# Optimization experiments

Hardware: AMD Instinct MI355X
Metric: run time of the kernel (lower is better)

## Reference

```python
import jax, jax.numpy as jnp
import numpy as np

N, C, H, W = 32, 512, 32, 32
K = 64  # num_clusters
D_OUT = 256


def _l2n(v, axis):
    # torch F.normalize: v / max(||v||, 1e-12)
    n = jnp.linalg.norm(v, axis=axis, keepdims=True)
    return v / jnp.maximum(n, 1e-12)


def _bn(v, gamma, beta):
    # BatchNorm1d, training mode (batch stats, biased variance), eps=1e-5
    m = v.mean(axis=0)
    var = ((v - m) ** 2).mean(axis=0)
    return (v - m) / jnp.sqrt(var + 1e-5) * gamma + beta


def setup_inputs() -> dict:
    key = jax.random.key(0)
    ks = jax.random.split(key, 5)
    x = jax.random.normal(ks[0], (N, C, H, W), dtype=jnp.float32)
    conv_w = jax.random.normal(ks[1], (K, C), dtype=jnp.float32) * 0.05
    centroids = jax.random.uniform(ks[2], (K, C), dtype=jnp.float32)
    hidden_w = jax.random.normal(ks[3], (K * C, D_OUT), dtype=jnp.float32) / jnp.sqrt(jnp.float32(C))
    gating_w = jax.random.normal(ks[4], (D_OUT, D_OUT), dtype=jnp.float32) / jnp.sqrt(jnp.float32(D_OUT))
    return {
        "x": x,
        "conv_w": conv_w,
        "centroids": centroids,
        "hidden_w": hidden_w,
        "bn2_gamma": jnp.ones((D_OUT,), jnp.float32),
        "bn2_beta": jnp.zeros((D_OUT,), jnp.float32),
        "gating_w": gating_w,
        "gbn_gamma": jnp.ones((D_OUT,), jnp.float32),
        "gbn_beta": jnp.zeros((D_OUT,), jnp.float32),
    }


def reference(x, conv_w, centroids, hidden_w, bn2_gamma, bn2_beta, gating_w, gbn_gamma, gbn_beta):
    n = x.shape[0]
    # descriptor-wise L2 normalization over channel dim
    x = _l2n(x, axis=1)                                  # [N,C,H,W]
    xf = x.reshape(n, x.shape[1], -1)                    # [N,C,S]
    # 1x1 conv -> soft assignment, softmax over clusters
    sa = jnp.einsum('ncs,kc->nks', xf, conv_w)           # [N,K,S]
    sa = jax.nn.softmax(sa, axis=1)
    # matmul-form NetVLAD: sum_s a[n,k,s]*(x[n,c,s]-cent[k,c])
    vlad = jnp.einsum('nks,ncs->nkc', sa, xf) \
         - sa.sum(axis=-1)[..., None] * centroids[None]  # [N,K,C]
    vlad = _l2n(vlad, axis=2)                            # intra-normalization
    vlad = _l2n(vlad.reshape(n, -1), axis=1)             # [N,K*C]
    v = vlad @ hidden_w                                  # [N,256]
    v = _bn(v, bn2_gamma, bn2_beta)
    # context gating
    gates = jax.nn.sigmoid(_bn(v @ gating_w, gbn_gamma, gbn_beta))
    return v * gates
```

## Files before the change

kernel.cpp:

```cpp
#include <hip/hip_runtime.h>
#include <math.h>

static constexpr int Nb = 32;
static constexpr int Cc = 512;
static constexpr int Ss = 1024;
static constexpr int Kk = 64;
static constexpr int Dd = 256;

typedef __attribute__((ext_vector_type(8))) short bf16x8;
typedef __attribute__((ext_vector_type(4))) float f32x4;
typedef __attribute__((ext_vector_type(4))) unsigned int u32x4;

union FragU { u32x4 u; bf16x8 h; };

__device__ __forceinline__ unsigned hi_pack(float x0, float x1) {
    return __builtin_amdgcn_perm(__float_as_uint(x1), __float_as_uint(x0), 0x07060302u);
}
__device__ __forceinline__ float trunc_hi(float x) {
    return __uint_as_float(__float_as_uint(x) & 0xFFFF0000u);
}
__device__ __forceinline__ void split8(const float* xv, FragU& bh, FragU& bl) {
#pragma unroll
    for (int p = 0; p < 4; ++p) {
        bh.u[p] = hi_pack(xv[2*p], xv[2*p+1]);
        float l0 = xv[2*p]   - trunc_hi(xv[2*p]);
        float l1 = xv[2*p+1] - trunc_hi(xv[2*p+1]);
        bl.u[p] = hi_pack(l0, l1);
    }
}

__device__ __forceinline__ void gload_lds16(const float* g, void* l) {
    __builtin_amdgcn_global_load_lds(
        (const __attribute__((address_space(1))) void*)g,
        (__attribute__((address_space(3))) void*)l, 16, 0, 0);
}

__global__ __launch_bounds__(256) void kprep_cw(
    const float* __restrict__ cw, short* __restrict__ cwh, short* __restrict__ cwl)
{
    int t = blockIdx.x * 256 + threadIdx.x;
    float4 v = *(const float4*)&cw[4 * (size_t)t];
    unsigned h0 = hi_pack(v.x, v.y), h1 = hi_pack(v.z, v.w);
    float l0 = v.x - trunc_hi(v.x), l1 = v.y - trunc_hi(v.y);
    float l2 = v.z - trunc_hi(v.z), l3 = v.w - trunc_hi(v.w);
    unsigned g0 = hi_pack(l0, l1), g1 = hi_pack(l2, l3);
    ((uint2*)cwh)[t] = make_uint2(h0, h1);
    ((uint2*)cwl)[t] = make_uint2(g0, g1);
}

__global__ __launch_bounds__(512) void k1_sa(
    const float* __restrict__ x, const short* __restrict__ cw_hi,
    const short* __restrict__ cw_lo, short* __restrict__ a_hi,
    short* __restrict__ a_lo, float* __restrict__ asum_part)
{
    __shared__ float xt[2 * 64 * 64];
    __shared__ f32x4 comb[4][64][4];
    __shared__ float combq[4][64];

    const int tid = threadIdx.x;
    const int w = tid >> 6, lane = tid & 63;
    const int wq = w & 3, wh = w >> 2;
    const int l15 = lane & 15, lg = lane >> 4;
    const int n = blockIdx.y, s0 = blockIdx.x * 64;

    const float* xg = x + ((size_t)n * Cc) * Ss + s0 + 4 * (tid & 15);
    const int st_c = tid >> 4;

    auto GL = [&](int b, int ct) {
#pragma unroll
        for (int r = 0; r < 2; ++r) {
            const float* src = xg + (size_t)(ct * 64 + st_c + 32 * r) * Ss;
            void* dst = (char*)xt + b * 16384 + 1024 * w + 8192 * r;
            gload_lds16(src, dst);
        }
    };

    f32x4 zero4 = {0.f, 0.f, 0.f, 0.f};
    f32x4 acc[4] = {zero4, zero4, zero4, zero4};
    float ssq = 0.f;

    const int sl = 16 * wq + l15;
    const int cb = wh * 32 + 8 * lg;

    GL(0, 0);
    __syncthreads();

    for (int ct = 0; ct < 8; ++ct) {
        const int b = ct & 1;
        if (ct < 7) GL(b ^ 1, ct + 1);

        float xv[8];
#pragma unroll
        for (int j = 0; j < 8; ++j) xv[j] = xt[b * 4096 + (cb + j) * 64 + sl];
#pragma unroll
        for (int j = 0; j < 8; ++j) ssq += xv[j] * xv[j];
        FragU bh, bl;
        split8(xv, bh, bl);

        const int cg = ct * 64 + cb;
#pragma unroll
        for (int m = 0; m < 4; ++m) {
            FragU ah, al;
            const int row = 16 * m + l15;
            ah.u = *(const u32x4*)&cw_hi[(size_t)row * Cc + cg];
            al.u = *(const u32x4*)&cw_lo[(size_t)row * Cc + cg];
            acc[m] = __builtin_amdgcn_mfma_f32_16x16x32_bf16(al.h, bh.h, acc[m], 0, 0, 0);
            acc[m] = __builtin_amdgcn_mfma_f32_16x16x32_bf16(ah.h, bl.h, acc[m], 0, 0, 0);
            acc[m] = __builtin_amdgcn_mfma_f32_16x16x32_bf16(ah.h, bh.h, acc[m], 0, 0, 0);
        }
        __syncthreads();
    }

    if (wh == 1) {
#pragma unroll
        for (int m = 0; m < 4; ++m) comb[wq][lane][m] = acc[m];
        combq[wq][lane] = ssq;
    }
    __syncthreads();
    if (wh == 1) return;

#pragma unroll
    for (int m = 0; m < 4; ++m) acc[m] += comb[wq][lane][m];
    ssq += combq[wq][lane];

    ssq += __shfl_xor(ssq, 16);
    ssq += __shfl_xor(ssq, 32);
    const float inv = 1.f / fmaxf(sqrtf(ssq), 1e-12f);

    float sv[4][4];
    float mmax = -1e30f;
#pragma unroll
    for (int m = 0; m < 4; ++m)
#pragma unroll
        for (int r = 0; r < 4; ++r) {
            sv[m][r] = acc[m][r] * inv;
            mmax = fmaxf(mmax, sv[m][r]);
        }
    mmax = fmaxf(mmax, __shfl_xor(mmax, 16));
    mmax = fmaxf(mmax, __shfl_xor(mmax, 32));
    float den = 0.f;
#pragma unroll
    for (int m = 0; m < 4; ++m)
#pragma unroll
        for (int r = 0; r < 4; ++r) {
            sv[m][r] = expf(sv[m][r] - mmax);
            den += sv[m][r];
        }
    den += __shfl_xor(den, 16);
    den += __shfl_xor(den, 32);
    const float rinv = 1.f / den;

    const int scol = s0 + sl;
#pragma unroll
    for (int m = 0; m < 4; ++m)
#pragma unroll
        for (int r = 0; r < 4; ++r) {
            const float a = sv[m][r] * rinv;
            const int k = 16 * m + 4 * lg + r;
            float t = a;
            t += __shfl_xor(t, 1); t += __shfl_xor(t, 2);
            t += __shfl_xor(t, 4); t += __shfl_xor(t, 8);
            if (l15 == 0)
                asum_part[((size_t)(n * Kk + k) << 6) + blockIdx.x * 4 + wq] = t;
            const float av = a * inv;
            const unsigned u = __float_as_uint(av);
            const float hv = __uint_as_float(u & 0xFFFF0000u);
            const size_t idx = (size_t)(n * Kk + k) * Ss + scol;
            a_hi[idx] = (short)(u >> 16);
            a_lo[idx] = (short)(__float_as_uint(av - hv) >> 16);
        }
}

__global__ __launch_bounds__(256) void kasum(
    const float* __restrict__ asum_part, float* __restrict__ asum)
{
    int row = blockIdx.x * 256 + threadIdx.x;
    const float* p = &asum_part[(size_t)row << 6];
    float s = 0.f;
#pragma unroll
    for (int i = 0; i < 16; ++i) {
        float4 v = *(const float4*)&p[4 * i];
        s += v.x + v.y + v.z + v.w;
    }
    asum[row] = s;
}

__global__ __launch_bounds__(512) void k2_vlad(
    const float* __restrict__ x, const short* __restrict__ a_hi,
    const short* __restrict__ a_lo, const float* __restrict__ centroids,
    const float* __restrict__ asum, float* __restrict__ vp0,
    float* __restrict__ vp1)
{
    __shared__ f32x4 comb[4][64][4];
    __shared__ float asum_l[64];

    const int tid = threadIdx.x;
    const int w = tid >> 6, lane = tid & 63;
    const int wq = w & 3, wh = w >> 2;
    const int l15 = lane & 15, lg = lane >> 4;
    const int n = blockIdx.x, cp = blockIdx.y, sh = blockIdx.z;

    if (sh == 1 && tid < 64) asum_l[tid] = asum[n * Kk + tid];

    f32x4 zero4 = {0.f, 0.f, 0.f, 0.f};
    f32x4 acc[4] = {zero4, zero4, zero4, zero4};

    const int c = cp * 64 + 16 * wq + l15;
    const int sbase = sh * 512 + wh * 256;
    const float* xrow = x + (size_t)(n * Cc + c) * Ss + sbase;
    const short* ahb = a_hi + (size_t)n * Kk * Ss + sbase;
    const short* alb = a_lo + (size_t)n * Kk * Ss + sbase;

#pragma unroll 2
    for (int st = 0; st < 8; ++st) {
        const int so = st * 32 + 8 * lg;
        float4 xa = *(const float4*)&xrow[so];
        float4 xb = *(const float4*)&xrow[so + 4];
        float xv[8] = {xa.x, xa.y, xa.z, xa.w, xb.x, xb.y, xb.z, xb.w};
        FragU bh, bl;
        split8(xv, bh, bl);
#pragma unroll
        for (int m = 0; m < 4; ++m) {
            FragU ah, al;
            const size_t ao = (size_t)(16 * m + l15) * Ss + so;
            ah.u = *(const u32x4*)&ahb[ao];
            al.u = *(const u32x4*)&alb[ao];
            acc[m] = __builtin_amdgcn_mfma_f32_16x16x32_bf16(al.h, bh.h, acc[m], 0, 0, 0);
            acc[m] = __builtin_amdgcn_mfma_f32_16x16x32_bf16(ah.h, bl.h, acc[m], 0, 0, 0);
            acc[m] = __builtin_amdgcn_mfma_f32_16x16x32_bf16(ah.h, bh.h, acc[m], 0, 0, 0);
        }
    }

    if (wh == 1) {
#pragma unroll
        for (int m = 0; m < 4; ++m) comb[wq][lane][m] = acc[m];
    }
    __syncthreads();
    if (wh == 1) return;

    float* dst = sh ? vp1 : vp0;
#pragma unroll
    for (int m = 0; m < 4; ++m) {
        acc[m] += comb[wq][lane][m];
#pragma unroll
        for (int r = 0; r < 4; ++r) {
            const int k = 16 * m + 4 * lg + r;
            float val = acc[m][r];
            if (sh == 1) val -= asum_l[k] * centroids[(size_t)k * Cc + c];
            dst[(size_t)(n * Kk + k) * Cc + c] = val;
        }
    }
}

__global__ __launch_bounds__(512) void k3a_norm(
    float* __restrict__ vlad, const float* __restrict__ vp1,
    float* __restrict__ nrm)
{
    const int tid = threadIdx.x;
    const int w = tid >> 6, lane = tid & 63;
    const int n = blockIdx.x, kg = blockIdx.y;
    const int row = (n * Kk) + kg * 8 + w;
    const size_t base = (size_t)row * Cc + lane * 8;

    float4 v0 = *(const float4*)&vlad[base];
    float4 v1 = *(const float4*)&vlad[base + 4];
    float4 u0 = *(const float4*)&vp1[base];
    float4 u1 = *(const float4*)&vp1[base + 4];
    v0.x += u0.x; v0.y += u0.y; v0.z += u0.z; v0.w += u0.w;
    v1.x += u1.x; v1.y += u1.y; v1.z += u1.z; v1.w += u1.w;
    *(float4*)&vlad[base] = v0;
    *(float4*)&vlad[base + 4] = v1;
    float ssq = v0.x*v0.x + v0.y*v0.y + v0.z*v0.z + v0.w*v0.w
              + v1.x*v1.x + v1.y*v1.y + v1.z*v1.z + v1.w*v1.w;
#pragma unroll
    for (int off = 32; off >= 1; off >>= 1) ssq += __shfl_xor(ssq, off);
    if (lane == 0) nrm[row] = sqrtf(ssq);
}

__global__ __launch_bounds__(64) void k3b_scale(
    const float* __restrict__ nrm, float* __restrict__ scale)
{
    const int n = blockIdx.x, k = threadIdx.x;
    float r = nrm[n * Kk + k];
    float rn = r / fmaxf(r, 1e-12f);
    float p = rn * rn;
#pragma unroll
    for (int off = 32; off >= 1; off >>= 1) p += __shfl_xor(p, off);
    float g = sqrtf(p);
    scale[n * Kk + k] = 1.f / (fmaxf(r, 1e-12f) * fmaxf(g, 1e-12f));
}

__global__ __launch_bounds__(512) void k4_hidden(
    const float* __restrict__ vlad, const float* __restrict__ scale,
    const float* __restrict__ hw, float* __restrict__ vpart)
{
    __shared__ float vl[128][36];
    __shared__ float scale_l[32];
    const int tid = threadIdx.x;
    const int kc0 = blockIdx.x * 128;
    const int k = kc0 >> 9;
    if (tid < 32) scale_l[tid] = scale[tid * Kk + k];
    __syncthreads();
#pragma unroll
    for (int i = 0; i < 8; ++i) {
        int idx = tid + i * 512;
        int nn = idx >> 7, kcl = idx & 127;
        vl[kcl][nn] = vlad[(size_t)nn * (Kk * Cc) + kc0 + kcl] * scale_l[nn];
    }
    __syncthreads();

    const int dq = tid & 63, nq = tid >> 6;
    float acc[4][4];
#pragma unroll
    for (int i = 0; i < 4; ++i)
#pragma unroll
        for (int j = 0; j < 4; ++j) acc[i][j] = 0.f;

    for (int kcl = 0; kcl < 128; ++kcl) {
        const float4 v0 = *(const float4*)&vl[kcl][nq * 4];
        const float* wrow = &hw[(size_t)(kc0 + kcl) * Dd + dq];
#pragma unroll
        for (int dd = 0; dd < 4; ++dd) {
            float w = wrow[64 * dd];
            acc[dd][0] += w * v0.x; acc[dd][1] += w * v0.y;
            acc[dd][2] += w * v0.z; acc[dd][3] += w * v0.w;
        }
    }
#pragma unroll
    for (int dd = 0; dd < 4; ++dd)
#pragma unroll
        for (int j = 0; j < 4; ++j)
            vpart[((size_t)blockIdx.x * Nb + nq * 4 + j) * Dd + dq + 64 * dd] = acc[dd][j];
}

__global__ __launch_bounds__(128) void k5a_reduce(
    const float* __restrict__ vpart, float* __restrict__ v)
{
    int flat = blockIdx.x * 128 + threadIdx.x;
    float s = 0.f;
#pragma unroll 8
    for (int ch = 0; ch < 256; ++ch) s += vpart[(size_t)ch * (Nb * Dd) + flat];
    v[flat] = s;
}

__global__ __launch_bounds__(256) void k5b_bn(
    const float* __restrict__ v, const float* __restrict__ gamma,
    const float* __restrict__ beta, float* __restrict__ v_bn)
{
    const int d = threadIdx.x;
    float vals[Nb];
    float s1 = 0.f;
#pragma unroll
    for (int n = 0; n < Nb; ++n) {
        vals[n] = v[n * Dd + d];
        s1 += vals[n];
    }
    float m = s1 * (1.f / Nb);
    float var = 0.f;
#pragma unroll
    for (int n = 0; n < Nb; ++n) {
        float t = vals[n] - m;
        var += t * t;
    }
    var *= (1.f / Nb);
    float inv = rsqrtf(var + 1e-5f);
    float g = gamma[d], b = beta[d];
#pragma unroll
    for (int n = 0; n < Nb; ++n)
        v_bn[n * Dd + d] = (vals[n] - m) * inv * g + b;
}

__global__ __launch_bounds__(256) void k5c_gate(
    const float* __restrict__ v_bn, const float* __restrict__ gw,
    float* __restrict__ g_raw)
{
    __shared__ float vb[Dd];
    const int n = blockIdx.x, d = threadIdx.x;
    vb[d] = v_bn[n * Dd + d];
    __syncthreads();
    float acc = 0.f;
#pragma unroll 8
    for (int c = 0; c < Dd; ++c) acc += vb[c] * gw[c * Dd + d];
    g_raw[n * Dd + d] = acc;
}

__global__ __launch_bounds__(256) void k5d_out(
    const float* __restrict__ g_raw, const float* __restrict__ v_bn,
    const float* __restrict__ ggamma, const float* __restrict__ gbeta,
    float* __restrict__ out)
{
    const int d = threadIdx.x;
    float vals[Nb];
    float s1 = 0.f;
#pragma unroll
    for (int n = 0; n < Nb; ++n) {
        vals[n] = g_raw[n * Dd + d];
        s1 += vals[n];
    }
    float m = s1 * (1.f / Nb);
    float var = 0.f;
#pragma unroll
    for (int n = 0; n < Nb; ++n) {
        float t = vals[n] - m;
        var += t * t;
    }
    var *= (1.f / Nb);
    float inv = rsqrtf(var + 1e-5f);
    float g = ggamma[d], b = gbeta[d];
#pragma unroll
    for (int n = 0; n < Nb; ++n) {
        float t = (vals[n] - m) * inv * g + b;
        float sg = 1.f / (1.f + expf(-t));
        out[n * Dd + d] = v_bn[n * Dd + d] * sg;
    }
}

extern "C" void kernel_launch(void* const* d_in, const int* in_sizes, int n_in,
                              void* d_out, int out_size, void* d_ws, size_t ws_size,
                              hipStream_t stream)
{
    const float* x         = (const float*)d_in[0];
    const float* conv_w    = (const float*)d_in[1];
    const float* centroids = (const float*)d_in[2];
    const float* hidden_w  = (const float*)d_in[3];
    const float* bn2_gamma = (const float*)d_in[4];
    const float* bn2_beta  = (const float*)d_in[5];
    const float* gating_w  = (const float*)d_in[6];
    const float* gbn_gamma = (const float*)d_in[7];
    const float* gbn_beta  = (const float*)d_in[8];
    float* out = (float*)d_out;

    char* B = (char*)d_ws;
    short* a_hi      = (short*)(B);
    short* a_lo      = (short*)(B + (4u << 20));
    float* vp0       = (float*)(B + (8u << 20));
    float* vp1       = (float*)(B + (12u << 20));
    short* cw_hi     = (short*)(B + (16u << 20));
    short* cw_lo     = (short*)(B + (16u << 20) + 65536u);
    float* asum_part = (float*)(B + (16u << 20) + 131072u);
    float* asum      = (float*)(B + (16u << 20) + 655360u);
    float* nrm       = asum + 2048;
    float* scale     = nrm + 2048;
    float* v         = scale + 2048;
    float* v_bn      = v + 8192;
    float* g_raw     = v_bn + 8192;
    float* vpart     = (float*)B;

    kprep_cw<<<32, 256, 0, stream>>>(conv_w, cw_hi, cw_lo);
    k1_sa<<<dim3(16, 32), 512, 0, stream>>>(x, cw_hi, cw_lo, a_hi, a_lo, asum_part);
    kasum<<<8, 256, 0, stream>>>(asum_part, asum);
    k2_vlad<<<dim3(32, 8, 2), 512, 0, stream>>>(x, a_hi, a_lo, centroids, asum, vp0, vp1);
    k3a_norm<<<dim3(32, 8), 512, 0, stream>>>(vp0, vp1, nrm);
    k3b_scale<<<32, 64, 0, stream>>>(nrm, scale);
    k4_hidden<<<256, 512, 0, stream>>>(vp0, scale, hidden_w, vpart);
    k5a_reduce<<<64, 128, 0, stream>>>(vpart, v);
    k5b_bn<<<1, 256, 0, stream>>>(v, bn2_gamma, bn2_beta, v_bn);
    k5c_gate<<<32, 256, 0, stream>>>(v_bn, gating_w, g_raw);
    k5d_out<<<1, 256, 0, stream>>>(g_raw, v_bn, gbn_gamma, gbn_beta, out);
}
```

Before: 143.6 us.

## Repartition soft-assignment and VLAD kernels for more blocks; fuse BN into gating GEMV

k1_sa now gives each block 32 spatial columns instead of 64, and each wave owns one 16-cluster row tile rather than all four. This doubles the grid, and the per-column softmax max and sum are combined across waves through shared memory. It adds an XOR swizzle on the LDS tile to avoid bank conflicts. k2_vlad takes 32 channels per block across 4 spatial slices, doubling its grid, and reduces three partial accumulators through LDS. The single-block BatchNorm kernel is folded into the gating GEMV, which removes one launch but has every block recompute the column statistics redundantly.

```diff
diff --git a/kernel.cpp b/kernel.cpp
--- a/kernel.cpp
+++ b/kernel.cpp
@@ -53,34 +53,31 @@
     const short* __restrict__ cw_lo, short* __restrict__ a_hi,
     short* __restrict__ a_lo, float* __restrict__ asum_part)
 {
-    __shared__ float xt[2 * 64 * 64];
-    __shared__ f32x4 comb[4][64][4];
-    __shared__ float combq[4][64];
+    __shared__ float xt[2 * 2048];
+    __shared__ float redm[4][32];
+    __shared__ float reds[4][32];
 
     const int tid = threadIdx.x;
     const int w = tid >> 6, lane = tid & 63;
-    const int wq = w & 3, wh = w >> 2;
+    const int m = w & 3, sg = w >> 2;
     const int l15 = lane & 15, lg = lane >> 4;
-    const int n = blockIdx.y, s0 = blockIdx.x * 64;
-
-    const float* xg = x + ((size_t)n * Cc) * Ss + s0 + 4 * (tid & 15);
-    const int st_c = tid >> 4;
+    const int n = blockIdx.y, s0 = blockIdx.x * 32;
+
+    const float* xg = x + (size_t)n * Cc * Ss + s0
+                    + 4 * ((tid & 7) ^ (4 * ((tid >> 6) & 1)));
+    const int st_c = tid >> 3;
 
     auto GL = [&](int b, int ct) {
-#pragma unroll
-        for (int r = 0; r < 2; ++r) {
-            const float* src = xg + (size_t)(ct * 64 + st_c + 32 * r) * Ss;
-            void* dst = (char*)xt + b * 16384 + 1024 * w + 8192 * r;
-            gload_lds16(src, dst);
-        }
+        const float* src = xg + (size_t)(ct * 64 + st_c) * Ss;
+        void* dst = (char*)xt + b * 8192 + 1024 * w;
+        gload_lds16(src, dst);
     };
 
-    f32x4 zero4 = {0.f, 0.f, 0.f, 0.f};
-    f32x4 acc[4] = {zero4, zero4, zero4, zero4};
+    f32x4 acc = {0.f, 0.f, 0.f, 0.f};
     float ssq = 0.f;
 
-    const int sl = 16 * wq + l15;
-    const int cb = wh * 32 + 8 * lg;
+    const int xcol = (16 * sg + l15) ^ (16 * (lg & 1));
+    const int row16 = 16 * m + l15;
 
     GL(0, 0);
     __syncthreads();
@@ -88,87 +85,75 @@
     for (int ct = 0; ct < 8; ++ct) {
         const int b = ct & 1;
         if (ct < 7) GL(b ^ 1, ct + 1);
-
-        float xv[8];
-#pragma unroll
-        for (int j = 0; j < 8; ++j) xv[j] = xt[b * 4096 + (cb + j) * 64 + sl];
-#pragma unroll
-        for (int j = 0; j < 8; ++j) ssq += xv[j] * xv[j];
-        FragU bh, bl;
-        split8(xv, bh, bl);
-
-        const int cg = ct * 64 + cb;
-#pragma unroll
-        for (int m = 0; m < 4; ++m) {
+#pragma unroll
+        for (int ks = 0; ks < 2; ++ks) {
+            const int cb = ks * 32 + 8 * lg;
+            float xv[8];
+#pragma unroll
+            for (int j = 0; j < 8; ++j) xv[j] = xt[b * 2048 + (cb + j) * 32 + xcol];
+#pragma unroll
+            for (int j = 0; j < 8; ++j) ssq += xv[j] * xv[j];
+            FragU bh, bl;
+            split8(xv, bh, bl);
             FragU ah, al;
-            const int row = 16 * m + l15;
-            ah.u = *(const u32x4*)&cw_hi[(size_t)row * Cc + cg];
-            al.u = *(const u32x4*)&cw_lo[(size_t)row * Cc + cg];
-            acc[m] = __builtin_amdgcn_mfma_f32_16x16x32_bf16(al.h, bh.h, acc[m], 0, 0, 0);
-            acc[m] = __builtin_amdgcn_mfma_f32_16x16x32_bf16(ah.h, bl.h, acc[m], 0, 0, 0);
-            acc[m] = __builtin_amdgcn_mfma_f32_16x16x32_bf16(ah.h, bh.h, acc[m], 0, 0, 0);
+            const int cg = ct * 64 + cb;
+            ah.u = *(const u32x4*)&cw_hi[(size_t)row16 * Cc + cg];
+            al.u = *(const u32x4*)&cw_lo[(size_t)row16 * Cc + cg];
+            acc = __builtin_amdgcn_mfma_f32_16x16x32_bf16(al.h, bh.h, acc, 0, 0, 0);
+            acc = __builtin_amdgcn_mfma_f32_16x16x32_bf16(ah.h, bl.h, acc, 0, 0, 0);
+            acc = __builtin_amdgcn_mfma_f32_16x16x32_bf16(ah.h, bh.h, acc, 0, 0, 0);
         }
         __syncthreads();
     }
-
-    if (wh == 1) {
-#pragma unroll
-        for (int m = 0; m < 4; ++m) comb[wq][lane][m] = acc[m];
-        combq[wq][lane] = ssq;
-    }
-    __syncthreads();
-    if (wh == 1) return;
-
-#pragma unroll
-    for (int m = 0; m < 4; ++m) acc[m] += comb[wq][lane][m];
-    ssq += combq[wq][lane];
 
     ssq += __shfl_xor(ssq, 16);
     ssq += __shfl_xor(ssq, 32);
     const float inv = 1.f / fmaxf(sqrtf(ssq), 1e-12f);
 
-    float sv[4][4];
+    const int sl = 16 * sg + l15;
+    float sv[4];
     float mmax = -1e30f;
 #pragma unroll
-    for (int m = 0; m < 4; ++m)
-#pragma unroll
-        for (int r = 0; r < 4; ++r) {
-            sv[m][r] = acc[m][r] * inv;
-            mmax = fmaxf(mmax, sv[m][r]);
-        }
+    for (int r = 0; r < 4; ++r) {
+        sv[r] = acc[r] * inv;
+        mmax = fmaxf(mmax, sv[r]);
+    }
     mmax = fmaxf(mmax, __shfl_xor(mmax, 16));
     mmax = fmaxf(mmax, __shfl_xor(mmax, 32));
+    if (lg == 0) redm[m][sl] = mmax;
+    __syncthreads();
+    mmax = fmaxf(fmaxf(redm[0][sl], redm[1][sl]),
+                 fmaxf(redm[2][sl], redm[3][sl]));
     float den = 0.f;
 #pragma unroll
-    for (int m = 0; m < 4; ++m)
-#pragma unroll
-        for (int r = 0; r < 4; ++r) {
-            sv[m][r] = expf(sv[m][r] - mmax);
-            den += sv[m][r];
-        }
+    for (int r = 0; r < 4; ++r) {
+        sv[r] = expf(sv[r] - mmax);
+        den += sv[r];
+    }
     den += __shfl_xor(den, 16);
     den += __shfl_xor(den, 32);
+    if (lg == 0) reds[m][sl] = den;
+    __syncthreads();
+    den = reds[0][sl] + reds[1][sl] + reds[2][sl] + reds[3][sl];
     const float rinv = 1.f / den;
 
     const int scol = s0 + sl;
 #pragma unroll
-    for (int m = 0; m < 4; ++m)
-#pragma unroll
-        for (int r = 0; r < 4; ++r) {
-            const float a = sv[m][r] * rinv;
-            const int k = 16 * m + 4 * lg + r;
-            float t = a;
-            t += __shfl_xor(t, 1); t += __shfl_xor(t, 2);
-            t += __shfl_xor(t, 4); t += __shfl_xor(t, 8);
-            if (l15 == 0)
-                asum_part[((size_t)(n * Kk + k) << 6) + blockIdx.x * 4 + wq] = t;
-            const float av = a * inv;
-            const unsigned u = __float_as_uint(av);
-            const float hv = __uint_as_float(u & 0xFFFF0000u);
-            const size_t idx = (size_t)(n * Kk + k) * Ss + scol;
-            a_hi[idx] = (short)(u >> 16);
-            a_lo[idx] = (short)(__float_as_uint(av - hv) >> 16);
-        }
+    for (int r = 0; r < 4; ++r) {
+        const float a = sv[r] * rinv;
+        const int k = 16 * m + 4 * lg + r;
+        float t = a;
+        t += __shfl_xor(t, 1); t += __shfl_xor(t, 2);
+        t += __shfl_xor(t, 4); t += __shfl_xor(t, 8);
+        if (l15 == 0)
+            asum_part[((size_t)(n * Kk + k) << 6) + blockIdx.x * 2 + sg] = t;
+        const float av = a * inv;
+        const unsigned u = __float_as_uint(av);
+        const float hv = __uint_as_float(u & 0xFFFF0000u);
+        const size_t idx = (size_t)(n * Kk + k) * Ss + scol;
+        a_hi[idx] = (short)(u >> 16);
+        a_lo[idx] = (short)(__float_as_uint(av - hv) >> 16);
+    }
 }
 
 __global__ __launch_bounds__(256) void kasum(
@@ -191,12 +176,12 @@
     const float* __restrict__ asum, float* __restrict__ vp0,
     float* __restrict__ vp1)
 {
-    __shared__ f32x4 comb[4][64][4];
+    __shared__ f32x4 comb[3][2][64][4];
     __shared__ float asum_l[64];
 
     const int tid = threadIdx.x;
     const int w = tid >> 6, lane = tid & 63;
-    const int wq = w & 3, wh = w >> 2;
+    const int wq = w & 1, wh = w >> 1;
     const int l15 = lane & 15, lg = lane >> 4;
     const int n = blockIdx.x, cp = blockIdx.y, sh = blockIdx.z;
 
@@ -205,14 +190,14 @@
     f32x4 zero4 = {0.f, 0.f, 0.f, 0.f};
     f32x4 acc[4] = {zero4, zero4, zero4, zero4};
 
-    const int c = cp * 64 + 16 * wq + l15;
-    const int sbase = sh * 512 + wh * 256;
+    const int c = cp * 32 + 16 * wq + l15;
+    const int sbase = sh * 512 + wh * 128;
     const float* xrow = x + (size_t)(n * Cc + c) * Ss + sbase;
     const short* ahb = a_hi + (size_t)n * Kk * Ss + sbase;
     const short* alb = a_lo + (size_t)n * Kk * Ss + sbase;
 
 #pragma unroll 2
-    for (int st = 0; st < 8; ++st) {
+    for (int st = 0; st < 4; ++st) {
         const int so = st * 32 + 8 * lg;
         float4 xa = *(const float4*)&xrow[so];
         float4 xb = *(const float4*)&xrow[so + 4];
@@ -231,17 +216,19 @@
         }
     }
 
-    if (wh == 1) {
-#pragma unroll
-        for (int m = 0; m < 4; ++m) comb[wq][lane][m] = acc[m];
-    }
-    __syncthreads();
-    if (wh == 1) return;
+    if (wh) {
+#pragma unroll
+        for (int m = 0; m < 4; ++m) comb[wh - 1][wq][lane][m] = acc[m];
+    }
+    __syncthreads();
+    if (wh) return;
 
     float* dst = sh ? vp1 : vp0;
 #pragma unroll
     for (int m = 0; m < 4; ++m) {
-        acc[m] += comb[wq][lane][m];
+        acc[m] += comb[0][wq][lane][m];
+        acc[m] += comb[1][wq][lane][m];
+        acc[m] += comb[2][wq][lane][m];
 #pragma unroll
         for (int r = 0; r < 4; ++r) {
             const int k = 16 * m + 4 * lg + r;
@@ -343,41 +330,31 @@
     v[flat] = s;
 }
 
-__global__ __launch_bounds__(256) void k5b_bn(
+__global__ __launch_bounds__(256) void k5bc_gate(
     const float* __restrict__ v, const float* __restrict__ gamma,
-    const float* __restrict__ beta, float* __restrict__ v_bn)
-{
-    const int d = threadIdx.x;
-    float vals[Nb];
+    const float* __restrict__ beta, const float* __restrict__ gw,
+    float* __restrict__ v_bn, float* __restrict__ g_raw)
+{
+    __shared__ float vb[Dd];
+    const int n = blockIdx.x, d = threadIdx.x;
+
     float s1 = 0.f;
-#pragma unroll
-    for (int n = 0; n < Nb; ++n) {
-        vals[n] = v[n * Dd + d];
-        s1 += vals[n];
-    }
-    float m = s1 * (1.f / Nb);
+#pragma unroll 8
+    for (int i = 0; i < Nb; ++i) s1 += v[i * Dd + d];
+    float mean = s1 * (1.f / Nb);
     float var = 0.f;
-#pragma unroll
-    for (int n = 0; n < Nb; ++n) {
-        float t = vals[n] - m;
+#pragma unroll 8
+    for (int i = 0; i < Nb; ++i) {
+        float t = v[i * Dd + d] - mean;
         var += t * t;
     }
     var *= (1.f / Nb);
     float inv = rsqrtf(var + 1e-5f);
-    float g = gamma[d], b = beta[d];
-#pragma unroll
-    for (int n = 0; n < Nb; ++n)
-        v_bn[n * Dd + d] = (vals[n] - m) * inv * g + b;
-}
-
-__global__ __launch_bounds__(256) void k5c_gate(
-    const float* __restrict__ v_bn, const float* __restrict__ gw,
-    float* __restrict__ g_raw)
-{
-    __shared__ float vb[Dd];
-    const int n = blockIdx.x, d = threadIdx.x;
-    vb[d] = v_bn[n * Dd + d];
-    __syncthreads();
+    float vbn = (v[n * Dd + d] - mean) * inv * gamma[d] + beta[d];
+    vb[d] = vbn;
+    v_bn[n * Dd + d] = vbn;
+    __syncthreads();
+
     float acc = 0.f;
 #pragma unroll 8
     for (int c = 0; c < Dd; ++c) acc += vb[c] * gw[c * Dd + d];
@@ -447,14 +424,13 @@
     float* vpart     = (float*)B;
 
     kprep_cw<<<32, 256, 0, stream>>>(conv_w, cw_hi, cw_lo);
-    k1_sa<<<dim3(16, 32), 512, 0, stream>>>(x, cw_hi, cw_lo, a_hi, a_lo, asum_part);
+    k1_sa<<<dim3(32, 32), 512, 0, stream>>>(x, cw_hi, cw_lo, a_hi, a_lo, asum_part);
     kasum<<<8, 256, 0, stream>>>(asum_part, asum);
-    k2_vlad<<<dim3(32, 8, 2), 512, 0, stream>>>(x, a_hi, a_lo, centroids, asum, vp0, vp1);
+    k2_vlad<<<dim3(32, 16, 2), 512, 0, stream>>>(x, a_hi, a_lo, centroids, asum, vp0, vp1);
     k3a_norm<<<dim3(32, 8), 512, 0, stream>>>(vp0, vp1, nrm);
     k3b_scale<<<32, 64, 0, stream>>>(nrm, scale);
     k4_hidden<<<256, 512, 0, stream>>>(vp0, scale, hidden_w, vpart);
     k5a_reduce<<<64, 128, 0, stream>>>(vpart, v);
-    k5b_bn<<<1, 256, 0, stream>>>(v, bn2_gamma, bn2_beta, v_bn);
-    k5c_gate<<<32, 256, 0, stream>>>(v_bn, gating_w, g_raw);
+    k5bc_gate<<<32, 256, 0, stream>>>(v, bn2_gamma, bn2_beta, gating_w, v_bn, g_raw);
     k5d_out<<<1, 256, 0, stream>>>(g_raw, v_bn, gbn_gamma, gbn_beta, out);
 }
```

Result: slower. 150.5 us (+4.8%).
